# Kernel tuning notes

Hardware: AMD Instinct MI355X
Metric: run time of the kernel (lower is better)

## Reference

```python
import jax, jax.numpy as jnp
import numpy as np

GAM1 = 1.0
GAM2 = 1.0
EPS = 0.01


def setup_inputs() -> dict:
    key = jax.random.key(0)
    k1, k2 = jax.random.split(key)
    m, p, k = 262144, 128, 10
    x = jax.random.normal(k1, (m, p), dtype=jnp.float32)
    y = jax.random.randint(k2, (m,), 0, k, dtype=jnp.int32)
    return {"x": x, "y": y, "num_classes": k}


def reference(x, y, num_classes):
    m, p = x.shape
    I = jnp.eye(p, dtype=x.dtype)
    scalar = p / (m * EPS)

    # W = x.T, so W @ W.T == x.T @ x  (p x p Gram)
    cov = x.T @ x
    discrimn_empi = jnp.linalg.slogdet(I + GAM1 * scalar * cov)[1] / 2.0
    discrimn_theo = jnp.linalg.slogdet(I + scalar * cov)[1] / 2.0

    # per-class compress loss: logdet(I + p/(n_j*eps) * W_j W_j^T) * n_j / m
    onehot = jax.nn.one_hot(y, num_classes, dtype=x.dtype)  # [m, k]
    counts = onehot.sum(axis=0)                             # [k]

    def class_cov(col):  # col: [m] 0/1 mask for one class
        return (x * col[:, None]).T @ x  # [p, p]

    covs = jax.lax.map(class_cov, onehot.T)  # [k, p, p], sequential over k classes

    safe_counts = jnp.maximum(counts, 1.0)
    scal = p / (safe_counts * EPS)                              # [k]
    lds = jnp.linalg.slogdet(I[None] + scal[:, None, None] * covs)[1]  # [k]
    compress = jnp.sum(jnp.where(counts > 0, lds * counts / m, 0.0)) / 2.0

    total_loss_empi = GAM2 * (-discrimn_empi) + compress
    return total_loss_empi, discrimn_empi, discrimn_theo, compress
```

## Files before the change

kernel.cpp:

```cpp
#include <hip/hip_runtime.h>

#define K 10
#define P 128
#define EPSV 0.01f
#define GAM1 1.0f
#define GAM2 1.0f
#define CH 256
#define SK 64
#define KS 68
#define SORTCH 2048
#define NTHR 256

typedef __attribute__((ext_vector_type(8))) short bf16x8;
typedef __attribute__((ext_vector_type(4))) short s16x4;
typedef __attribute__((ext_vector_type(4))) float f32x4;

static __device__ __forceinline__ short f2bf(float f) {
    unsigned u = __float_as_uint(f);
    u = (u + 0x7FFFu + ((u >> 16) & 1u)) >> 16;
    return (short)u;
}

static __device__ __forceinline__ float rdlane(float v, int srclane) {
    return __int_as_float(__builtin_amdgcn_readlane(__float_as_int(v), srclane));
}

__global__ void hist_kernel(const int* __restrict__ y, int* __restrict__ blk_counts, int m) {
    __shared__ int h[K];
    int t = threadIdx.x;
    if (t < K) h[t] = 0;
    __syncthreads();
    int base = blockIdx.x * SORTCH;
    int rows = min(SORTCH, m - base);
    for (int i = t; i < rows; i += NTHR) atomicAdd(&h[y[base + i]], 1);
    __syncthreads();
    if (t < K) blk_counts[blockIdx.x * K + t] = h[t];
}

__global__ void scan_kernel(const int* __restrict__ blk_counts, int* __restrict__ blk_offsets,
                            int* __restrict__ counts, int* __restrict__ pstart, int nb) {
    __shared__ int s[K][128];
    __shared__ int sps[K + 1];
    int t = threadIdx.x;
    int own[K];
    if (t < 128) {
        for (int c = 0; c < K; ++c) {
            int v = (t < nb) ? blk_counts[t * K + c] : 0;
            own[c] = v;
            s[c][t] = v;
        }
    }
    __syncthreads();
    for (int off = 1; off < 128; off <<= 1) {
        int tmp[K];
        if (t < 128)
            for (int c = 0; c < K; ++c) tmp[c] = (t >= off) ? s[c][t - off] : 0;
        __syncthreads();
        if (t < 128)
            for (int c = 0; c < K; ++c) s[c][t] += tmp[c];
        __syncthreads();
    }
    if (t == 0) {
        int run = 0;
        for (int c = 0; c < K; ++c) {
            sps[c] = run;
            int tot = s[c][127];
            counts[c] = tot;
            pstart[c] = run;
            run += ((tot + CH - 1) / CH) * CH;
        }
        sps[K] = run;
        pstart[K] = run;
    }
    __syncthreads();
    if (t < nb)
        for (int c = 0; c < K; ++c)
            blk_offsets[t * K + c] = sps[c] + s[c][t] - own[c];
}

__global__ void scatter_kernel(const int* __restrict__ y, const int* __restrict__ blk_offsets,
                               int* __restrict__ perm, int m) {
    __shared__ int cur[K];
    int t = threadIdx.x;
    if (t < K) cur[t] = blk_offsets[blockIdx.x * K + t];
    __syncthreads();
    int base = blockIdx.x * SORTCH;
    int rows = min(SORTCH, m - base);
    for (int i = t; i < rows; i += NTHR) {
        int row = base + i;
        int pos = atomicAdd(&cur[y[row]], 1);
        perm[pos] = row;
    }
}

__global__ __launch_bounds__(NTHR) void gram_kernel(const float* __restrict__ x,
                                                    const int* __restrict__ perm,
                                                    float* __restrict__ partials) {
    __shared__ int pm[CH];
    __shared__ short xsT[2][P * KS];
    int t = threadIdx.x;
    for (int i = t; i < CH; i += NTHR) pm[i] = perm[(size_t)blockIdx.x * CH + i];

    const int lane = t & 63;
    const int wave = t >> 6;
    const int m16 = lane & 15;
    const int quad = lane >> 4;
    const int wr = wave >> 1;
    const int wc = wave & 1;
    const int c2 = t & 63;
    const int rg = t >> 6;

    f32x4 acc[4][4];
#pragma unroll
    for (int a = 0; a < 4; ++a)
#pragma unroll
        for (int b = 0; b < 4; ++b) acc[a][b] = (f32x4){0.f, 0.f, 0.f, 0.f};

    __syncthreads();

    float2 v[16];
#define LOAD_STAGE(S)                                                          \
    {                                                                          \
        int sb = (S)*SK;                                                       \
        _Pragma("unroll") for (int ii = 0; ii < 16; ++ii) {                    \
            int r = pm[sb + rg * 16 + ii];                                     \
            if (r >= 0) v[ii] = ((const float2*)(x + (size_t)r * P))[c2];      \
            else { v[ii].x = 0.f; v[ii].y = 0.f; }                             \
        }                                                                      \
    }

    LOAD_STAGE(0)
    for (int s = 0; s < CH / SK; ++s) {
        const int buf = s & 1;
        short b0[16], b1[16];
#pragma unroll
        for (int ii = 0; ii < 16; ++ii) { b0[ii] = f2bf(v[ii].x); b1[ii] = f2bf(v[ii].y); }
        int col0 = 2 * c2, col1 = 2 * c2 + 1;
#pragma unroll
        for (int q = 0; q < 4; ++q) {
            s16x4 w0 = {b0[q * 4], b0[q * 4 + 1], b0[q * 4 + 2], b0[q * 4 + 3]};
            s16x4 w1 = {b1[q * 4], b1[q * 4 + 1], b1[q * 4 + 2], b1[q * 4 + 3]};
            *(s16x4*)&xsT[buf][col0 * KS + rg * 16 + q * 4] = w0;
            *(s16x4*)&xsT[buf][col1 * KS + rg * 16 + q * 4] = w1;
        }
        __syncthreads();
        if (s < CH / SK - 1) LOAD_STAGE(s + 1)
#pragma unroll
        for (int kk = 0; kk < 2; ++kk) {
            int k0 = kk * 32 + quad * 8;
            bf16x8 af[4], bfr[4];
#pragma unroll
            for (int a = 0; a < 4; ++a) {
                int colA = wr * 64 + a * 16 + m16;
                union { bf16x8 v8; s16x4 h[2]; } u;
                u.h[0] = *(s16x4*)&xsT[buf][colA * KS + k0];
                u.h[1] = *(s16x4*)&xsT[buf][colA * KS + k0 + 4];
                af[a] = u.v8;
            }
#pragma unroll
            for (int b = 0; b < 4; ++b) {
                int colB = wc * 64 + b * 16 + m16;
                union { bf16x8 v8; s16x4 h[2]; } u;
                u.h[0] = *(s16x4*)&xsT[buf][colB * KS + k0];
                u.h[1] = *(s16x4*)&xsT[buf][colB * KS + k0 + 4];
                bfr[b] = u.v8;
            }
#pragma unroll
            for (int a = 0; a < 4; ++a)
#pragma unroll
                for (int b = 0; b < 4; ++b)
                    acc[a][b] = __builtin_amdgcn_mfma_f32_16x16x32_bf16(af[a], bfr[b], acc[a][b], 0, 0, 0);
        }
    }
#undef LOAD_STAGE
    float* out = partials + (size_t)blockIdx.x * P * P;
#pragma unroll
    for (int a = 0; a < 4; ++a)
#pragma unroll
        for (int b = 0; b < 4; ++b)
#pragma unroll
            for (int r = 0; r < 4; ++r) {
                int gi = wr * 64 + a * 16 + quad * 4 + r;
                int gj = wc * 64 + b * 16 + m16;
                out[gi * P + gj] = acc[a][b][r];
            }
}

__global__ __launch_bounds__(256) void reduce_kernel(const float* __restrict__ partials,
                                                     const int* __restrict__ pstart,
                                                     float* __restrict__ grams, int nbg) {
    int c = blockIdx.x >> 6;
    int idx = ((blockIdx.x & 63) << 8) | threadIdx.x;
    int b0 = pstart[c] / CH;
    int b1 = (c == K - 1) ? nbg : (pstart[c + 1] / CH);
    float s0 = 0.f, s1 = 0.f, s2 = 0.f, s3 = 0.f;
    int b = b0;
    for (; b + 3 < b1; b += 4) {
        s0 += partials[(size_t)(b + 0) * P * P + idx];
        s1 += partials[(size_t)(b + 1) * P * P + idx];
        s2 += partials[(size_t)(b + 2) * P * P + idx];
        s3 += partials[(size_t)(b + 3) * P * P + idx];
    }
    for (; b < b1; ++b) s0 += partials[(size_t)b * P * P + idx];
    grams[c * P * P + idx] = (s0 + s1) + (s2 + s3);
}

__global__ void sum_kernel(const float* __restrict__ grams, float* __restrict__ gsum) {
    int idx = blockIdx.x * 256 + threadIdx.x;
    float s = 0.f;
#pragma unroll
    for (int c = 0; c < K; ++c) s += grams[c * P * P + idx];
    gsum[idx] = s;
}

__global__ __launch_bounds__(256, 1) void logdet_kernel(const float* __restrict__ grams,
                                                        const float* __restrict__ gsum,
                                                        const int* __restrict__ counts,
                                                        float* __restrict__ logd, int m) {
    __shared__ float A[P * P];
    int t = threadIdx.x, b = blockIdx.x;
    float scale;
    if (b == 0) scale = GAM1 * (float)P / ((float)m * EPSV);
    else if (b == 1) scale = (float)P / ((float)m * EPSV);
    else {
        float cnt = (float)counts[b - 2];
        if (cnt < 1.f) cnt = 1.f;
        scale = (float)P / (cnt * EPSV);
    }
    const float* src = (b < 2) ? gsum : (grams + (size_t)(b - 2) * P * P);
    for (int idx = t; idx < P * P; idx += 256) {
        int i = idx >> 7, c = idx & (P - 1);
        A[idx] = scale * src[idx] + ((i == c) ? 1.f : 0.f);
    }
    __syncthreads();

    const int lane = t & 63;
    const int wid = t >> 6;
    float lsum = 0.f;

    for (int bs = 0; bs < 4; ++bs) {
        const int j0 = bs * 32;
        if (wid == 0) {
            float a[32];
            if (lane < 32) {
#pragma unroll
                for (int cc = 0; cc < 8; ++cc)
                    *(f32x4*)&a[cc * 4] = *(f32x4*)&A[(j0 + lane) * P + j0 + cc * 4];
            } else {
#pragma unroll
                for (int cc = 0; cc < 32; ++cc) a[cc] = 0.f;
            }
            float myinv = 0.f;
#pragma unroll
            for (int tt = 0; tt < 32; ++tt) {
                float utt = rdlane(a[tt], tt);
                float inv = __builtin_amdgcn_rcpf(utt);
                lsum += __logf(utt);
                if (lane == tt) myinv = inv;
                bool act = (lane < 32) && (lane > tt);
                float lm = act ? a[tt] * inv : 0.f;
                if (act) a[tt] = lm;
#pragma unroll
                for (int k2 = tt + 1; k2 < 32; ++k2) {
                    float utk = rdlane(a[k2], tt);
                    a[k2] -= lm * utk;
                }
            }
            if (lane < 32) A[(j0 + lane) * P + j0 + lane] = myinv;

            if (bs < 3) {
                int nc = P - j0 - 32;
                int c0 = j0 + 32 + lane;
                int c1 = c0 + 64;
                bool v0 = lane < nc;
                bool v1 = lane + 64 < nc;
                int c0a = v0 ? c0 : (j0 + 32);
                int c1a = v1 ? c1 : (j0 + 32);
                float ua[32], ub[32];
#pragma unroll
                for (int j = 0; j < 32; ++j) {
                    ua[j] = A[(j0 + j) * P + c0a];
                    ub[j] = A[(j0 + j) * P + c1a];
                }
#pragma unroll
                for (int j = 0; j < 32; ++j) {
#pragma unroll
                    for (int t2 = 0; t2 < j; ++t2) {
                        float ljt = rdlane(a[t2], j);
                        ua[j] -= ljt * ua[t2];
                        ub[j] -= ljt * ub[t2];
                    }
                }
#pragma unroll
                for (int j = 0; j < 32; ++j) {
                    if (v0) A[(j0 + j) * P + c0] = ua[j];
                    if (v1) A[(j0 + j) * P + c1] = ub[j];
                }
            }
        }
        __syncthreads();

        if (bs < 3) {
            int nc = P - j0 - 32;
            int nt = nc >> 2;
            int ntiles = nt * nt;
            for (int tile = t; tile < ntiles; tile += 256) {
                int ti = tile / nt, tk = tile - ti * nt;
                int i0 = j0 + 32 + ti * 4, k0 = j0 + 32 + tk * 4;
                f32x4 acc0 = {0, 0, 0, 0}, acc1 = {0, 0, 0, 0};
                f32x4 acc2 = {0, 0, 0, 0}, acc3 = {0, 0, 0, 0};
#pragma unroll
                for (int j = 0; j < 32; ++j) {
                    const float* row = &A[(j0 + j) * P];
                    float invd = row[j0 + j];
                    f32x4 ui = *(const f32x4*)&row[i0];
                    f32x4 uk = *(const f32x4*)&row[k0];
                    uk *= invd;
                    acc0 += ui[0] * uk;
                    acc1 += ui[1] * uk;
                    acc2 += ui[2] * uk;
                    acc3 += ui[3] * uk;
                }
                f32x4* r0 = (f32x4*)&A[(i0 + 0) * P + k0];
                f32x4* r1 = (f32x4*)&A[(i0 + 1) * P + k0];
                f32x4* r2 = (f32x4*)&A[(i0 + 2) * P + k0];
                f32x4* r3 = (f32x4*)&A[(i0 + 3) * P + k0];
                *r0 -= acc0; *r1 -= acc1; *r2 -= acc2; *r3 -= acc3;
            }
            __syncthreads();
        }
    }
    if (t == 0) logd[b] = lsum;
}

__global__ void final_kernel(const float* __restrict__ logd, const int* __restrict__ counts,
                             float* __restrict__ out, int m) {
    if (threadIdx.x == 0 && blockIdx.x == 0) {
        float empi = 0.5f * logd[0];
        float theo = 0.5f * logd[1];
        float comp = 0.f;
        for (int c = 0; c < K; ++c) {
            float cnt = (float)counts[c];
            if (cnt > 0.f) comp += logd[2 + c] * cnt / (float)m;
        }
        comp *= 0.5f;
        out[0] = GAM2 * (-empi) + comp;
        out[1] = empi;
        out[2] = theo;
        out[3] = comp;
    }
}

extern "C" void kernel_launch(void* const* d_in, const int* in_sizes, int n_in,
                              void* d_out, int out_size, void* d_ws, size_t ws_size,
                              hipStream_t stream) {
    const float* x = (const float*)d_in[0];
    const int* y = (const int*)d_in[1];
    int m = in_sizes[1];
    int nbs = (m + SORTCH - 1) / SORTCH;
    int nbg = (m + CH - 1) / CH + K;

    char* ws = (char*)d_ws;
    float* grams = (float*)ws;
    float* gsum = (float*)(ws + 655360);
    float* logd = (float*)(ws + 720896);
    int* counts = (int*)(ws + 720960);
    int* pstart = (int*)(ws + 721024);
    int* blk_counts = (int*)(ws + 721152);
    int* blk_offsets = (int*)(ws + 726272);
    int* perm = (int*)(ws + 731392);
    float* partials = (float*)(ws + 1802240);

    hipMemsetAsync(perm, 0xFF, (size_t)nbg * CH * 4, stream);

    hist_kernel<<<nbs, NTHR, 0, stream>>>(y, blk_counts, m);
    scan_kernel<<<1, NTHR, 0, stream>>>(blk_counts, blk_offsets, counts, pstart, nbs);
    scatter_kernel<<<nbs, NTHR, 0, stream>>>(y, blk_offsets, perm, m);
    gram_kernel<<<nbg, NTHR, 0, stream>>>(x, perm, partials);
    reduce_kernel<<<K * 64, 256, 0, stream>>>(partials, pstart, grams, nbg);
    sum_kernel<<<P * P / 256, 256, 0, stream>>>(grams, gsum);
    logdet_kernel<<<K + 2, 256, 0, stream>>>(grams, gsum, counts, logd, m);
    final_kernel<<<1, 1, 0, stream>>>(logd, counts, (float*)d_out, m);
}
```

Before: 301.9 us.

## Fuse sum/final kernels into logdet, drop perm memset, double gram chunk size

Removes the perm memset by computing each gram block's valid row count from pstart/counts, folds the class-sum into the logdet load and the final combination into logdet via atomics (zeroing the output in hist_kernel). Doubles CH to halve partial Gram writes and the reduction work, and vectorizes the reduce kernel with float4 loads. Trades fewer launches and less partial traffic for fewer gram blocks (less parallelism) and atomic output accumulation, whose floating-point summation order is nondeterministic.

```diff
diff --git a/kernel.cpp b/kernel.cpp
--- a/kernel.cpp
+++ b/kernel.cpp
@@ -5,7 +5,7 @@
 #define EPSV 0.01f
 #define GAM1 1.0f
 #define GAM2 1.0f
-#define CH 256
+#define CH 512
 #define SK 64
 #define KS 68
 #define SORTCH 2048
@@ -25,9 +25,11 @@
     return __int_as_float(__builtin_amdgcn_readlane(__float_as_int(v), srclane));
 }
 
-__global__ void hist_kernel(const int* __restrict__ y, int* __restrict__ blk_counts, int m) {
+__global__ void hist_kernel(const int* __restrict__ y, int* __restrict__ blk_counts,
+                            float* __restrict__ out, int m) {
     __shared__ int h[K];
     int t = threadIdx.x;
+    if (blockIdx.x == 0 && t < 4) out[t] = 0.f;
     if (t < K) h[t] = 0;
     __syncthreads();
     int base = blockIdx.x * SORTCH;
@@ -95,11 +97,19 @@
 
 __global__ __launch_bounds__(NTHR) void gram_kernel(const float* __restrict__ x,
                                                     const int* __restrict__ perm,
+                                                    const int* __restrict__ counts,
+                                                    const int* __restrict__ pstart,
                                                     float* __restrict__ partials) {
     __shared__ int pm[CH];
     __shared__ short xsT[2][P * KS];
     int t = threadIdx.x;
-    for (int i = t; i < CH; i += NTHR) pm[i] = perm[(size_t)blockIdx.x * CH + i];
+    int base = blockIdx.x * CH;
+    int cls = 0;
+#pragma unroll
+    for (int c = 1; c < K; ++c)
+        if (base >= pstart[c]) cls = c;
+    const int nvalid = pstart[cls] + counts[cls] - base;
+    for (int i = t; i < CH; i += NTHR) pm[i] = perm[base + i];
 
     const int lane = t & 63;
     const int wave = t >> 6;
@@ -123,9 +133,11 @@
     {                                                                          \
         int sb = (S)*SK;                                                       \
         _Pragma("unroll") for (int ii = 0; ii < 16; ++ii) {                    \
-            int r = pm[sb + rg * 16 + ii];                                     \
-            if (r >= 0) v[ii] = ((const float2*)(x + (size_t)r * P))[c2];      \
-            else { v[ii].x = 0.f; v[ii].y = 0.f; }                             \
+            int ri = sb + rg * 16 + ii;                                        \
+            if (ri < nvalid) {                                                 \
+                int r = pm[ri];                                                \
+                v[ii] = ((const float2*)(x + (size_t)r * P))[c2];              \
+            } else { v[ii].x = 0.f; v[ii].y = 0.f; }                           \
         }                                                                      \
     }
 
@@ -189,34 +201,27 @@
 __global__ __launch_bounds__(256) void reduce_kernel(const float* __restrict__ partials,
                                                      const int* __restrict__ pstart,
                                                      float* __restrict__ grams, int nbg) {
-    int c = blockIdx.x >> 6;
-    int idx = ((blockIdx.x & 63) << 8) | threadIdx.x;
+    int c = blockIdx.x >> 4;
+    int e4 = ((blockIdx.x & 15) << 8) | threadIdx.x;
+    const f32x4* p4 = (const f32x4*)partials;
     int b0 = pstart[c] / CH;
     int b1 = (c == K - 1) ? nbg : (pstart[c + 1] / CH);
-    float s0 = 0.f, s1 = 0.f, s2 = 0.f, s3 = 0.f;
+    f32x4 s0 = {0, 0, 0, 0}, s1 = {0, 0, 0, 0}, s2 = {0, 0, 0, 0}, s3 = {0, 0, 0, 0};
     int b = b0;
+    const int Q = P * P / 4;
     for (; b + 3 < b1; b += 4) {
-        s0 += partials[(size_t)(b + 0) * P * P + idx];
-        s1 += partials[(size_t)(b + 1) * P * P + idx];
-        s2 += partials[(size_t)(b + 2) * P * P + idx];
-        s3 += partials[(size_t)(b + 3) * P * P + idx];
-    }
-    for (; b < b1; ++b) s0 += partials[(size_t)b * P * P + idx];
-    grams[c * P * P + idx] = (s0 + s1) + (s2 + s3);
-}
-
-__global__ void sum_kernel(const float* __restrict__ grams, float* __restrict__ gsum) {
-    int idx = blockIdx.x * 256 + threadIdx.x;
-    float s = 0.f;
-#pragma unroll
-    for (int c = 0; c < K; ++c) s += grams[c * P * P + idx];
-    gsum[idx] = s;
+        s0 += p4[(size_t)(b + 0) * Q + e4];
+        s1 += p4[(size_t)(b + 1) * Q + e4];
+        s2 += p4[(size_t)(b + 2) * Q + e4];
+        s3 += p4[(size_t)(b + 3) * Q + e4];
+    }
+    for (; b < b1; ++b) s0 += p4[(size_t)b * Q + e4];
+    ((f32x4*)grams)[c * Q + e4] = (s0 + s1) + (s2 + s3);
 }
 
 __global__ __launch_bounds__(256, 1) void logdet_kernel(const float* __restrict__ grams,
-                                                        const float* __restrict__ gsum,
                                                         const int* __restrict__ counts,
-                                                        float* __restrict__ logd, int m) {
+                                                        float* __restrict__ out, int m) {
     __shared__ float A[P * P];
     int t = threadIdx.x, b = blockIdx.x;
     float scale;
@@ -227,10 +232,18 @@
         if (cnt < 1.f) cnt = 1.f;
         scale = (float)P / (cnt * EPSV);
     }
-    const float* src = (b < 2) ? gsum : (grams + (size_t)(b - 2) * P * P);
     for (int idx = t; idx < P * P; idx += 256) {
         int i = idx >> 7, c = idx & (P - 1);
-        A[idx] = scale * src[idx] + ((i == c) ? 1.f : 0.f);
+        float g;
+        if (b < 2) {
+            float ssum = 0.f;
+#pragma unroll
+            for (int cc = 0; cc < K; ++cc) ssum += grams[cc * P * P + idx];
+            g = ssum;
+        } else {
+            g = grams[(size_t)(b - 2) * P * P + idx];
+        }
+        A[idx] = scale * g + ((i == c) ? 1.f : 0.f);
     }
     __syncthreads();
 
@@ -330,24 +343,19 @@
             __syncthreads();
         }
     }
-    if (t == 0) logd[b] = lsum;
-}
-
-__global__ void final_kernel(const float* __restrict__ logd, const int* __restrict__ counts,
-                             float* __restrict__ out, int m) {
-    if (threadIdx.x == 0 && blockIdx.x == 0) {
-        float empi = 0.5f * logd[0];
-        float theo = 0.5f * logd[1];
-        float comp = 0.f;
-        for (int c = 0; c < K; ++c) {
-            float cnt = (float)counts[c];
-            if (cnt > 0.f) comp += logd[2 + c] * cnt / (float)m;
-        }
-        comp *= 0.5f;
-        out[0] = GAM2 * (-empi) + comp;
-        out[1] = empi;
-        out[2] = theo;
-        out[3] = comp;
+    if (t == 0) {
+        if (b == 0) {
+            float empi = 0.5f * lsum;
+            out[1] = empi;
+            atomicAdd(&out[0], GAM2 * (-empi));
+        } else if (b == 1) {
+            out[2] = 0.5f * lsum;
+        } else {
+            float cnt = (float)counts[b - 2];
+            float val = 0.5f * lsum * cnt / (float)m;
+            atomicAdd(&out[0], val);
+            atomicAdd(&out[3], val);
+        }
     }
 }
 
@@ -362,23 +370,17 @@
 
     char* ws = (char*)d_ws;
     float* grams = (float*)ws;
-    float* gsum = (float*)(ws + 655360);
-    float* logd = (float*)(ws + 720896);
-    int* counts = (int*)(ws + 720960);
-    int* pstart = (int*)(ws + 721024);
-    int* blk_counts = (int*)(ws + 721152);
-    int* blk_offsets = (int*)(ws + 726272);
-    int* perm = (int*)(ws + 731392);
-    float* partials = (float*)(ws + 1802240);
-
-    hipMemsetAsync(perm, 0xFF, (size_t)nbg * CH * 4, stream);
-
-    hist_kernel<<<nbs, NTHR, 0, stream>>>(y, blk_counts, m);
+    int* counts = (int*)(ws + 655360);
+    int* pstart = (int*)(ws + 655424);
+    int* blk_counts = (int*)(ws + 655488);
+    int* blk_offsets = (int*)(ws + 660608);
+    int* perm = (int*)(ws + 665728);
+    float* partials = (float*)(ws + 1769472);
+
+    hist_kernel<<<nbs, NTHR, 0, stream>>>(y, blk_counts, (float*)d_out, m);
     scan_kernel<<<1, NTHR, 0, stream>>>(blk_counts, blk_offsets, counts, pstart, nbs);
     scatter_kernel<<<nbs, NTHR, 0, stream>>>(y, blk_offsets, perm, m);
-    gram_kernel<<<nbg, NTHR, 0, stream>>>(x, perm, partials);
-    reduce_kernel<<<K * 64, 256, 0, stream>>>(partials, pstart, grams, nbg);
-    sum_kernel<<<P * P / 256, 256, 0, stream>>>(grams, gsum);
-    logdet_kernel<<<K + 2, 256, 0, stream>>>(grams, gsum, counts, logd, m);
-    final_kernel<<<1, 1, 0, stream>>>(logd, counts, (float*)d_out, m);
-}
+    gram_kernel<<<nbg, NTHR, 0, stream>>>(x, perm, counts, pstart, partials);
+    reduce_kernel<<<K * 16, 256, 0, stream>>>(partials, pstart, grams, nbg);
+    logdet_kernel<<<K + 2, 256, 0, stream>>>(grams, counts, (float*)d_out, m);
+}
```

After: 321.0 us. 1.06x slower.
